# Performance work log

Hardware: AMD Instinct MI355X
Metric: run time of the kernel (lower is better)

## Reference

```python
import jax, jax.numpy as jnp
import numpy as np

B, E, H, C, R = 16, 1024, 1024, 64, 64  # batch, input_size, hidden_size, context_size, context_rank
H4 = 4 * H


def setup_inputs() -> dict:
    key = jax.random.key(0)
    ks = jax.random.split(key, 12)
    n = lambda k, shape, scale: jax.random.normal(k, shape, dtype=jnp.float32) * scale
    return {
        'x': n(ks[0], (B, E), 1.0),
        'h': n(ks[1], (B, H), 1.0),
        'c': n(ks[2], (B, H), 1.0),
        'context': n(ks[3], (B, C), 1.0),
        'Wi': n(ks[4], (E, H4), 0.02),
        'Wi_b': n(ks[5], (H4,), 0.02),
        'Wh': n(ks[6], (H, H4), 0.02),
        'Wh_b': n(ks[7], (H4,), 0.02),
        'AZ_il': n(ks[8], (C, E, R), 0.02),
        'AZ_ir': n(ks[9], (R, H4, C), 0.02),
        'AZ_hl': n(ks[10], (C, H, R), 0.02),
        'AZ_hr': n(ks[11], (R, H4, C), 0.02),
    }


def reference(x, h, c, context, Wi, Wi_b, Wh, Wh_b, AZ_il, AZ_ir, AZ_hl, AZ_hr):
    hs = Wh.shape[0]
    # compute_context_weights: per-sample low-rank weight perturbations
    lhs_i = jnp.einsum('bc,cer->ber', context, AZ_il)      # [B,E,R]
    rhs_i = jnp.einsum('bc,rjc->brj', context, AZ_ir)      # [B,R,4H]
    A_i = jnp.einsum('ber,brj->bej', lhs_i, rhs_i)         # [B,E,4H]
    lhs_h = jnp.einsum('bc,chr->bhr', context, AZ_hl)      # [B,H,R]
    rhs_h = jnp.einsum('bc,rjc->brj', context, AZ_hr)      # [B,R,4H]
    A_h = jnp.einsum('bhr,brj->bhj', lhs_h, rhs_h)         # [B,H,4H]
    # forward (faithful to original: context weights are multiplied by 0)
    Wi_eff = 0.0 * A_i + Wi                                # [B,E,4H]
    Wh_eff = 0.0 * A_h + Wh                                # [B,H,4H]
    ifgo = (jnp.einsum('be,bej->bj', x, Wi_eff) + Wi_b
            + jnp.einsum('bh,bhj->bj', h, Wh_eff) + Wh_b)  # [B,4H]
    i = jax.nn.sigmoid(ifgo[:, :hs])
    f = jax.nn.sigmoid(ifgo[:, hs:2 * hs])
    g = jnp.tanh(ifgo[:, 2 * hs:3 * hs])
    o = jax.nn.sigmoid(ifgo[:, 3 * hs:])
    c_new = f * c + i * g
    h_new = o * jnp.tanh(c_new)
    return (h_new, c_new)
```

## Files before the change

### kernel.cpp

```cpp
#include <hip/hip_runtime.h>
#include <stdint.h>

#define H4_ 4096
#define B_  16

__global__ __launch_bounds__(256) void k1_gemm(
    const float* __restrict__ x, const float* __restrict__ h,
    const float* __restrict__ Wi, const float* __restrict__ Wh,
    float* __restrict__ part, int chunks)
{
    __shared__ float a_lds[256][16];
    __shared__ float red[8][16][32];

    const int ct = blockIdx.x & 127;
    const int s  = blockIdx.x >> 7;
    const int j0 = ct * 32;
    const int t  = threadIdx.x;
    const int c8 = t & 7;
    const int bq = (t >> 3) & 3;
    const int ks = t >> 5;

    float acc[4][4];
    #pragma unroll
    for (int r = 0; r < 4; r++)
        #pragma unroll
        for (int c = 0; c < 4; c++) acc[r][c] = 0.f;

    const int m_beg = s * chunks, m_end = m_beg + chunks;
    for (int m = m_beg; m < m_end; ++m) {
        const float* A  = (m < 4) ? x : h;
        const float* W  = (m < 4) ? Wi : Wh;
        const int    e0 = (m & 3) * 256;

        {
            const int b = t & 15, kc = t >> 4;
            const float* src = A + b * 1024 + e0 + kc * 16;
            float4 v0 = *(const float4*)(src);
            float4 v1 = *(const float4*)(src + 4);
            float4 v2 = *(const float4*)(src + 8);
            float4 v3 = *(const float4*)(src + 12);
            const float vv[16] = { v0.x, v0.y, v0.z, v0.w, v1.x, v1.y, v1.z, v1.w,
                                   v2.x, v2.y, v2.z, v2.w, v3.x, v3.y, v3.z, v3.w };
            #pragma unroll
            for (int j = 0; j < 16; j++) a_lds[kc * 16 + j][b] = vv[j];
        }
        __syncthreads();

        const float* wp = W + (size_t)e0 * H4_ + j0 + c8 * 4;
        #pragma unroll 8
        for (int i = 0; i < 32; i++) {
            const int kl = ks * 32 + i;
            float4 w = *(const float4*)(wp + (size_t)kl * H4_);
            float4 a = *(const float4*)&a_lds[kl][bq * 4];
            acc[0][0] += a.x * w.x; acc[0][1] += a.x * w.y; acc[0][2] += a.x * w.z; acc[0][3] += a.x * w.w;
            acc[1][0] += a.y * w.x; acc[1][1] += a.y * w.y; acc[1][2] += a.y * w.z; acc[1][3] += a.y * w.w;
            acc[2][0] += a.z * w.x; acc[2][1] += a.z * w.y; acc[2][2] += a.z * w.z; acc[2][3] += a.z * w.w;
            acc[3][0] += a.w * w.x; acc[3][1] += a.w * w.y; acc[3][2] += a.w * w.z; acc[3][3] += a.w * w.w;
        }
        __syncthreads();
    }

    #pragma unroll
    for (int r = 0; r < 4; r++)
        *(float4*)&red[ks][bq * 4 + r][c8 * 4] =
            make_float4(acc[r][0], acc[r][1], acc[r][2], acc[r][3]);
    __syncthreads();
    {
        const int b = t >> 4, c = t & 15;
        float s0 = 0.f, s1 = 0.f;
        #pragma unroll
        for (int kk = 0; kk < 8; kk++) {
            s0 += red[kk][b][c];
            s1 += red[kk][b][c + 16];
        }
        float* dst = part + ((size_t)s * B_ + b) * H4_ + j0;
        dst[c]      = s0;
        dst[c + 16] = s1;
    }
}

__global__ __launch_bounds__(256) void k2_act(
    const float* __restrict__ part, const float* __restrict__ c,
    const float* __restrict__ Wi_b, const float* __restrict__ Wh_b,
    float* __restrict__ out, int split)
{
    const int tg = blockIdx.x * 256 + threadIdx.x;
    const int b  = tg >> 10;
    const int j  = tg & 1023;

    float g4[4];
    #pragma unroll
    for (int g = 0; g < 4; g++) {
        const int col = g * 1024 + j;
        float acc = Wi_b[col] + Wh_b[col];
        for (int ss = 0; ss < split; ss++)
            acc += part[((size_t)ss * B_ + b) * H4_ + col];
        g4[g] = acc;
    }
    const float ig = 1.f / (1.f + __expf(-g4[0]));
    const float fg = 1.f / (1.f + __expf(-g4[1]));
    const float gg = tanhf(g4[2]);
    const float og = 1.f / (1.f + __expf(-g4[3]));
    const float cv = c[tg];
    const float cn = fg * cv + ig * gg;
    const float hn = og * tanhf(cn);
    out[tg]         = hn;
    out[16384 + tg] = cn;
}

__global__ __launch_bounds__(256) void k_fused(
    const float* __restrict__ x, const float* __restrict__ h,
    const float* __restrict__ cin,
    const float* __restrict__ Wi, const float* __restrict__ Wh,
    const float* __restrict__ Wi_b, const float* __restrict__ Wh_b,
    float* __restrict__ out)
{
    __shared__ float a_lds[256][16];
    __shared__ float red[16][16][16];
    __shared__ float gate_s[4][16][16];

    const int j0 = blockIdx.x * 16;
    const int t  = threadIdx.x;
    const int ks = t >> 4;
    const int bq = (t >> 2) & 3;
    const int c4 = t & 3;

    float acc[4][4][4];
    #pragma unroll
    for (int g = 0; g < 4; g++)
        #pragma unroll
        for (int r = 0; r < 4; r++)
            #pragma unroll
            for (int c = 0; c < 4; c++) acc[g][r][c] = 0.f;

    for (int m = 0; m < 8; ++m) {
        const float* A  = (m < 4) ? x : h;
        const float* W  = (m < 4) ? Wi : Wh;
        const int    e0 = (m & 3) * 256;
        {
            const int b = t & 15, kc = t >> 4;
            const float* src = A + b * 1024 + e0 + kc * 16;
            float4 v0 = *(const float4*)(src);
            float4 v1 = *(const float4*)(src + 4);
            float4 v2 = *(const float4*)(src + 8);
            float4 v3 = *(const float4*)(src + 12);
            const float vv[16] = { v0.x, v0.y, v0.z, v0.w, v1.x, v1.y, v1.z, v1.w,
                                   v2.x, v2.y, v2.z, v2.w, v3.x, v3.y, v3.z, v3.w };
            #pragma unroll
            for (int jj = 0; jj < 16; jj++) a_lds[kc * 16 + jj][b] = vv[jj];
        }
        __syncthreads();
        #pragma unroll 4
        for (int i = 0; i < 16; i++) {
            const int kl = ks * 16 + i;
            float4 a = *(const float4*)&a_lds[kl][bq * 4];
            const float av[4] = { a.x, a.y, a.z, a.w };
            #pragma unroll
            for (int g = 0; g < 4; g++) {
                float4 w = *(const float4*)(W + (size_t)(e0 + kl) * H4_ + g * 1024 + j0 + c4 * 4);
                #pragma unroll
                for (int r = 0; r < 4; r++) {
                    acc[g][r][0] += av[r] * w.x; acc[g][r][1] += av[r] * w.y;
                    acc[g][r][2] += av[r] * w.z; acc[g][r][3] += av[r] * w.w;
                }
            }
        }
        __syncthreads();
    }

    #pragma unroll
    for (int g = 0; g < 4; g++) {
        #pragma unroll
        for (int r = 0; r < 4; r++)
            *(float4*)&red[ks][bq * 4 + r][c4 * 4] =
                make_float4(acc[g][r][0], acc[g][r][1], acc[g][r][2], acc[g][r][3]);
        __syncthreads();
        {
            const int b = t >> 4, c = t & 15;
            float sum = 0.f;
            #pragma unroll
            for (int kk = 0; kk < 16; kk++) sum += red[kk][b][c];
            gate_s[g][b][c] = sum;
        }
        __syncthreads();
    }

    {
        const int b = t >> 4, jj = t & 15;
        const int j = j0 + jj;
        const float s0 = gate_s[0][b][jj] + Wi_b[j]        + Wh_b[j];
        const float s1 = gate_s[1][b][jj] + Wi_b[1024 + j] + Wh_b[1024 + j];
        const float s2 = gate_s[2][b][jj] + Wi_b[2048 + j] + Wh_b[2048 + j];
        const float s3 = gate_s[3][b][jj] + Wi_b[3072 + j] + Wh_b[3072 + j];
        const float ig = 1.f / (1.f + __expf(-s0));
        const float fg = 1.f / (1.f + __expf(-s1));
        const float gg = tanhf(s2);
        const float og = 1.f / (1.f + __expf(-s3));
        const float cv = cin[b * 1024 + j];
        const float cn = fg * cv + ig * gg;
        const float hn = og * tanhf(cn);
        out[b * 1024 + j]         = hn;
        out[16384 + b * 1024 + j] = cn;
    }
}

extern "C" void kernel_launch(void* const* d_in, const int* in_sizes, int n_in,
                              void* d_out, int out_size, void* d_ws, size_t ws_size,
                              hipStream_t stream) {
    (void)in_sizes; (void)n_in; (void)out_size;
    const float* x    = (const float*)d_in[0];
    const float* h    = (const float*)d_in[1];
    const float* c    = (const float*)d_in[2];
    const float* Wi   = (const float*)d_in[4];
    const float* Wi_b = (const float*)d_in[5];
    const float* Wh   = (const float*)d_in[6];
    const float* Wh_b = (const float*)d_in[7];

    float* part = (float*)d_ws;
    float* out  = (float*)d_out;

    const size_t need1 = (size_t)B_ * H4_ * sizeof(float);
    int split = 0;
    if      (ws_size >= 4 * need1) split = 4;
    else if (ws_size >= 2 * need1) split = 2;
    else if (ws_size >= 1 * need1) split = 1;

    if (split > 0) {
        k1_gemm<<<128 * split, 256, 0, stream>>>(x, h, Wi, Wh, part, 8 / split);
        k2_act<<<64, 256, 0, stream>>>(part, c, Wi_b, Wh_b, out, split);
    } else {
        k_fused<<<64, 256, 0, stream>>>(x, h, c, Wi, Wh, Wi_b, Wh_b, out);
    }
}
```

Measured before the change: 186.1 us.

## Fuse GEMM and LSTM gate activation into one 256-block kernel

Replaces the split-K two-kernel path (partial GEMM sums to workspace, then an activation kernel) with a single fused kernel over 256 blocks. Each block owns 4 hidden columns across all four gates, so the gate nonlinearities and cell update run in-block after an LDS reduction. This removes the workspace round trip and the second launch. In exchange, each block streams the full K=2048 reduction, and each thread reads a 16-byte segment per gate (4 floats per row per gate), which may coalesce less well than before.

```diff
diff --git a/kernel.cpp b/kernel.cpp
--- a/kernel.cpp
+++ b/kernel.cpp
@@ -4,21 +4,23 @@
 #define H4_ 4096
 #define B_  16
 
-__global__ __launch_bounds__(256) void k1_gemm(
+__global__ __launch_bounds__(256) void k_fused2(
     const float* __restrict__ x, const float* __restrict__ h,
+    const float* __restrict__ cin,
     const float* __restrict__ Wi, const float* __restrict__ Wh,
-    float* __restrict__ part, int chunks)
+    const float* __restrict__ Wi_b, const float* __restrict__ Wh_b,
+    float* __restrict__ out)
 {
     __shared__ float a_lds[256][16];
-    __shared__ float red[8][16][32];
+    __shared__ float red[16][16][16];
+    __shared__ float gsum[16][16];
 
-    const int ct = blockIdx.x & 127;
-    const int s  = blockIdx.x >> 7;
-    const int j0 = ct * 32;
+    const int bl = blockIdx.x;
+    const int j0 = (bl & 7) * 128 + (bl >> 3) * 4;
     const int t  = threadIdx.x;
-    const int c8 = t & 7;
-    const int bq = (t >> 3) & 3;
-    const int ks = t >> 5;
+    const int g  = t & 3;
+    const int bq = (t >> 2) & 3;
+    const int ks = t >> 4;
 
     float acc[4][4];
     #pragma unroll
@@ -26,8 +28,7 @@
         #pragma unroll
         for (int c = 0; c < 4; c++) acc[r][c] = 0.f;
 
-    const int m_beg = s * chunks, m_end = m_beg + chunks;
-    for (int m = m_beg; m < m_end; ++m) {
+    for (int m = 0; m < 8; ++m) {
         const float* A  = (m < 4) ? x : h;
         const float* W  = (m < 4) ? Wi : Wh;
         const int    e0 = (m & 3) * 256;
@@ -46,10 +47,10 @@
         }
         __syncthreads();
 
-        const float* wp = W + (size_t)e0 * H4_ + j0 + c8 * 4;
-        #pragma unroll 8
-        for (int i = 0; i < 32; i++) {
-            const int kl = ks * 32 + i;
+        const float* wp = W + (size_t)e0 * H4_ + g * 1024 + j0;
+        #pragma unroll
+        for (int i = 0; i < 16; i++) {
+            const int kl = ks * 16 + i;
             float4 w = *(const float4*)(wp + (size_t)kl * H4_);
             float4 a = *(const float4*)&a_lds[kl][bq * 4];
             acc[0][0] += a.x * w.x; acc[0][1] += a.x * w.y; acc[0][2] += a.x * w.z; acc[0][3] += a.x * w.w;
@@ -62,136 +63,25 @@
 
     #pragma unroll
     for (int r = 0; r < 4; r++)
-        *(float4*)&red[ks][bq * 4 + r][c8 * 4] =
+        *(float4*)&red[ks][bq * 4 + r][g * 4] =
             make_float4(acc[r][0], acc[r][1], acc[r][2], acc[r][3]);
     __syncthreads();
     {
-        const int b = t >> 4, c = t & 15;
-        float s0 = 0.f, s1 = 0.f;
+        const int b = t >> 4, c16 = t & 15;
+        float s = 0.f;
         #pragma unroll
-        for (int kk = 0; kk < 8; kk++) {
-            s0 += red[kk][b][c];
-            s1 += red[kk][b][c + 16];
-        }
-        float* dst = part + ((size_t)s * B_ + b) * H4_ + j0;
-        dst[c]      = s0;
-        dst[c + 16] = s1;
+        for (int kk = 0; kk < 16; kk++) s += red[kk][b][c16];
+        gsum[b][c16] = s;
     }
-}
+    __syncthreads();
 
-__global__ __launch_bounds__(256) void k2_act(
-    const float* __restrict__ part, const float* __restrict__ c,
-    const float* __restrict__ Wi_b, const float* __restrict__ Wh_b,
-    float* __restrict__ out, int split)
-{
-    const int tg = blockIdx.x * 256 + threadIdx.x;
-    const int b  = tg >> 10;
-    const int j  = tg & 1023;
-
-    float g4[4];
-    #pragma unroll
-    for (int g = 0; g < 4; g++) {
-        const int col = g * 1024 + j;
-        float acc = Wi_b[col] + Wh_b[col];
-        for (int ss = 0; ss < split; ss++)
-            acc += part[((size_t)ss * B_ + b) * H4_ + col];
-        g4[g] = acc;
-    }
-    const float ig = 1.f / (1.f + __expf(-g4[0]));
-    const float fg = 1.f / (1.f + __expf(-g4[1]));
-    const float gg = tanhf(g4[2]);
-    const float og = 1.f / (1.f + __expf(-g4[3]));
-    const float cv = c[tg];
-    const float cn = fg * cv + ig * gg;
-    const float hn = og * tanhf(cn);
-    out[tg]         = hn;
-    out[16384 + tg] = cn;
-}
-
-__global__ __launch_bounds__(256) void k_fused(
-    const float* __restrict__ x, const float* __restrict__ h,
-    const float* __restrict__ cin,
-    const float* __restrict__ Wi, const float* __restrict__ Wh,
-    const float* __restrict__ Wi_b, const float* __restrict__ Wh_b,
-    float* __restrict__ out)
-{
-    __shared__ float a_lds[256][16];
-    __shared__ float red[16][16][16];
-    __shared__ float gate_s[4][16][16];
-
-    const int j0 = blockIdx.x * 16;
-    const int t  = threadIdx.x;
-    const int ks = t >> 4;
-    const int bq = (t >> 2) & 3;
-    const int c4 = t & 3;
-
-    float acc[4][4][4];
-    #pragma unroll
-    for (int g = 0; g < 4; g++)
-        #pragma unroll
-        for (int r = 0; r < 4; r++)
-            #pragma unroll
-            for (int c = 0; c < 4; c++) acc[g][r][c] = 0.f;
-
-    for (int m = 0; m < 8; ++m) {
-        const float* A  = (m < 4) ? x : h;
-        const float* W  = (m < 4) ? Wi : Wh;
-        const int    e0 = (m & 3) * 256;
-        {
-            const int b = t & 15, kc = t >> 4;
-            const float* src = A + b * 1024 + e0 + kc * 16;
-            float4 v0 = *(const float4*)(src);
-            float4 v1 = *(const float4*)(src + 4);
-            float4 v2 = *(const float4*)(src + 8);
-            float4 v3 = *(const float4*)(src + 12);
-            const float vv[16] = { v0.x, v0.y, v0.z, v0.w, v1.x, v1.y, v1.z, v1.w,
-                                   v2.x, v2.y, v2.z, v2.w, v3.x, v3.y, v3.z, v3.w };
-            #pragma unroll
-            for (int jj = 0; jj < 16; jj++) a_lds[kc * 16 + jj][b] = vv[jj];
-        }
-        __syncthreads();
-        #pragma unroll 4
-        for (int i = 0; i < 16; i++) {
-            const int kl = ks * 16 + i;
-            float4 a = *(const float4*)&a_lds[kl][bq * 4];
-            const float av[4] = { a.x, a.y, a.z, a.w };
-            #pragma unroll
-            for (int g = 0; g < 4; g++) {
-                float4 w = *(const float4*)(W + (size_t)(e0 + kl) * H4_ + g * 1024 + j0 + c4 * 4);
-                #pragma unroll
-                for (int r = 0; r < 4; r++) {
-                    acc[g][r][0] += av[r] * w.x; acc[g][r][1] += av[r] * w.y;
-                    acc[g][r][2] += av[r] * w.z; acc[g][r][3] += av[r] * w.w;
-                }
-            }
-        }
-        __syncthreads();
-    }
-
-    #pragma unroll
-    for (int g = 0; g < 4; g++) {
-        #pragma unroll
-        for (int r = 0; r < 4; r++)
-            *(float4*)&red[ks][bq * 4 + r][c4 * 4] =
-                make_float4(acc[g][r][0], acc[g][r][1], acc[g][r][2], acc[g][r][3]);
-        __syncthreads();
-        {
-            const int b = t >> 4, c = t & 15;
-            float sum = 0.f;
-            #pragma unroll
-            for (int kk = 0; kk < 16; kk++) sum += red[kk][b][c];
-            gate_s[g][b][c] = sum;
-        }
-        __syncthreads();
-    }
-
-    {
-        const int b = t >> 4, jj = t & 15;
+    if (t < 64) {
+        const int b = t >> 2, jj = t & 3;
         const int j = j0 + jj;
-        const float s0 = gate_s[0][b][jj] + Wi_b[j]        + Wh_b[j];
-        const float s1 = gate_s[1][b][jj] + Wi_b[1024 + j] + Wh_b[1024 + j];
-        const float s2 = gate_s[2][b][jj] + Wi_b[2048 + j] + Wh_b[2048 + j];
-        const float s3 = gate_s[3][b][jj] + Wi_b[3072 + j] + Wh_b[3072 + j];
+        const float s0 = gsum[b][jj]      + Wi_b[j]        + Wh_b[j];
+        const float s1 = gsum[b][4 + jj]  + Wi_b[1024 + j] + Wh_b[1024 + j];
+        const float s2 = gsum[b][8 + jj]  + Wi_b[2048 + j] + Wh_b[2048 + j];
+        const float s3 = gsum[b][12 + jj] + Wi_b[3072 + j] + Wh_b[3072 + j];
         const float ig = 1.f / (1.f + __expf(-s0));
         const float fg = 1.f / (1.f + __expf(-s1));
         const float gg = tanhf(s2);
@@ -207,7 +97,7 @@
 extern "C" void kernel_launch(void* const* d_in, const int* in_sizes, int n_in,
                               void* d_out, int out_size, void* d_ws, size_t ws_size,
                               hipStream_t stream) {
-    (void)in_sizes; (void)n_in; (void)out_size;
+    (void)in_sizes; (void)n_in; (void)out_size; (void)d_ws; (void)ws_size;
     const float* x    = (const float*)d_in[0];
     const float* h    = (const float*)d_in[1];
     const float* c    = (const float*)d_in[2];
@@ -216,19 +106,6 @@
     const float* Wh   = (const float*)d_in[6];
     const float* Wh_b = (const float*)d_in[7];
 
-    float* part = (float*)d_ws;
-    float* out  = (float*)d_out;
-
-    const size_t need1 = (size_t)B_ * H4_ * sizeof(float);
-    int split = 0;
-    if      (ws_size >= 4 * need1) split = 4;
-    else if (ws_size >= 2 * need1) split = 2;
-    else if (ws_size >= 1 * need1) split = 1;
-
-    if (split > 0) {
-        k1_gemm<<<128 * split, 256, 0, stream>>>(x, h, Wi, Wh, part, 8 / split);
-        k2_act<<<64, 256, 0, stream>>>(part, c, Wi_b, Wh_b, out, split);
-    } else {
-        k_fused<<<64, 256, 0, stream>>>(x, h, c, Wi, Wh, Wi_b, Wh_b, out);
-    }
+    k_fused2<<<256, 256, 0, stream>>>(x, h, c, Wi, Wh, Wi_b, Wh_b,
+                                      (float*)d_out);
 }
```

After: 202.3 us. +8.7%, slower.

## Split K eight ways across 1024 blocks and widen fused fallback grid

Applied to the files above, without the earlier changes.

The split-K GEMM now always uses eight K-chunks, one 256-row slab per block, launched as 1024 blocks with the split index in the low bits of blockIdx. This raises parallelism for the memory-bound weight stream, and the activation kernel now sums a fixed, unrolled eight partials. The fused fallback is restructured to 256 blocks of four columns per gate. The cost is a larger workspace requirement (8x partials) and more partial-sum traffic in the second kernel. If the workspace is too small, the code now falls back to the fused kernel instead of using fewer splits.

```diff
diff --git a/kernel.cpp b/kernel.cpp
--- a/kernel.cpp
+++ b/kernel.cpp
@@ -7,13 +7,13 @@
 __global__ __launch_bounds__(256) void k1_gemm(
     const float* __restrict__ x, const float* __restrict__ h,
     const float* __restrict__ Wi, const float* __restrict__ Wh,
-    float* __restrict__ part, int chunks)
+    float* __restrict__ part)
 {
     __shared__ float a_lds[256][16];
     __shared__ float red[8][16][32];
 
-    const int ct = blockIdx.x & 127;
-    const int s  = blockIdx.x >> 7;
+    const int s  = blockIdx.x & 7;
+    const int ct = blockIdx.x >> 3;
     const int j0 = ct * 32;
     const int t  = threadIdx.x;
     const int c8 = t & 7;
@@ -26,38 +26,34 @@
         #pragma unroll
         for (int c = 0; c < 4; c++) acc[r][c] = 0.f;
 
-    const int m_beg = s * chunks, m_end = m_beg + chunks;
-    for (int m = m_beg; m < m_end; ++m) {
-        const float* A  = (m < 4) ? x : h;
-        const float* W  = (m < 4) ? Wi : Wh;
-        const int    e0 = (m & 3) * 256;
-
-        {
-            const int b = t & 15, kc = t >> 4;
-            const float* src = A + b * 1024 + e0 + kc * 16;
-            float4 v0 = *(const float4*)(src);
-            float4 v1 = *(const float4*)(src + 4);
-            float4 v2 = *(const float4*)(src + 8);
-            float4 v3 = *(const float4*)(src + 12);
-            const float vv[16] = { v0.x, v0.y, v0.z, v0.w, v1.x, v1.y, v1.z, v1.w,
-                                   v2.x, v2.y, v2.z, v2.w, v3.x, v3.y, v3.z, v3.w };
-            #pragma unroll
-            for (int j = 0; j < 16; j++) a_lds[kc * 16 + j][b] = vv[j];
-        }
-        __syncthreads();
-
-        const float* wp = W + (size_t)e0 * H4_ + j0 + c8 * 4;
-        #pragma unroll 8
-        for (int i = 0; i < 32; i++) {
-            const int kl = ks * 32 + i;
-            float4 w = *(const float4*)(wp + (size_t)kl * H4_);
-            float4 a = *(const float4*)&a_lds[kl][bq * 4];
-            acc[0][0] += a.x * w.x; acc[0][1] += a.x * w.y; acc[0][2] += a.x * w.z; acc[0][3] += a.x * w.w;
-            acc[1][0] += a.y * w.x; acc[1][1] += a.y * w.y; acc[1][2] += a.y * w.z; acc[1][3] += a.y * w.w;
-            acc[2][0] += a.z * w.x; acc[2][1] += a.z * w.y; acc[2][2] += a.z * w.z; acc[2][3] += a.z * w.w;
-            acc[3][0] += a.w * w.x; acc[3][1] += a.w * w.y; acc[3][2] += a.w * w.z; acc[3][3] += a.w * w.w;
-        }
-        __syncthreads();
+    const float* A  = (s < 4) ? x : h;
+    const float* W  = (s < 4) ? Wi : Wh;
+    const int    e0 = (s & 3) * 256;
+
+    {
+        const int b = t & 15, kc = t >> 4;
+        const float* src = A + b * 1024 + e0 + kc * 16;
+        float4 v0 = *(const float4*)(src);
+        float4 v1 = *(const float4*)(src + 4);
+        float4 v2 = *(const float4*)(src + 8);
+        float4 v3 = *(const float4*)(src + 12);
+        const float vv[16] = { v0.x, v0.y, v0.z, v0.w, v1.x, v1.y, v1.z, v1.w,
+                               v2.x, v2.y, v2.z, v2.w, v3.x, v3.y, v3.z, v3.w };
+        #pragma unroll
+        for (int j = 0; j < 16; j++) a_lds[kc * 16 + j][b] = vv[j];
+    }
+    __syncthreads();
+
+    const float* wp = W + (size_t)e0 * H4_ + j0 + c8 * 4;
+    #pragma unroll 8
+    for (int i = 0; i < 32; i++) {
+        const int kl = ks * 32 + i;
+        float4 w = *(const float4*)(wp + (size_t)kl * H4_);
+        float4 a = *(const float4*)&a_lds[kl][bq * 4];
+        acc[0][0] += a.x * w.x; acc[0][1] += a.x * w.y; acc[0][2] += a.x * w.z; acc[0][3] += a.x * w.w;
+        acc[1][0] += a.y * w.x; acc[1][1] += a.y * w.y; acc[1][2] += a.y * w.z; acc[1][3] += a.y * w.w;
+        acc[2][0] += a.z * w.x; acc[2][1] += a.z * w.y; acc[2][2] += a.z * w.z; acc[2][3] += a.z * w.w;
+        acc[3][0] += a.w * w.x; acc[3][1] += a.w * w.y; acc[3][2] += a.w * w.z; acc[3][3] += a.w * w.w;
     }
 
     #pragma unroll
@@ -82,7 +78,7 @@
 __global__ __launch_bounds__(256) void k2_act(
     const float* __restrict__ part, const float* __restrict__ c,
     const float* __restrict__ Wi_b, const float* __restrict__ Wh_b,
-    float* __restrict__ out, int split)
+    float* __restrict__ out)
 {
     const int tg = blockIdx.x * 256 + threadIdx.x;
     const int b  = tg >> 10;
@@ -93,7 +89,8 @@
     for (int g = 0; g < 4; g++) {
         const int col = g * 1024 + j;
         float acc = Wi_b[col] + Wh_b[col];
-        for (int ss = 0; ss < split; ss++)
+        #pragma unroll
+        for (int ss = 0; ss < 8; ss++)
             acc += part[((size_t)ss * B_ + b) * H4_ + col];
         g4[g] = acc;
     }
@@ -108,7 +105,7 @@
     out[16384 + tg] = cn;
 }
 
-__global__ __launch_bounds__(256) void k_fused(
+__global__ __launch_bounds__(256) void k_fused2(
     const float* __restrict__ x, const float* __restrict__ h,
     const float* __restrict__ cin,
     const float* __restrict__ Wi, const float* __restrict__ Wh,
@@ -117,21 +114,20 @@
 {
     __shared__ float a_lds[256][16];
     __shared__ float red[16][16][16];
-    __shared__ float gate_s[4][16][16];
-
-    const int j0 = blockIdx.x * 16;
+    __shared__ float gsum[16][16];
+
+    const int bl = blockIdx.x;
+    const int j0 = (bl & 7) * 128 + (bl >> 3) * 4;
     const int t  = threadIdx.x;
+    const int g  = t & 3;
+    const int bq = (t >> 2) & 3;
     const int ks = t >> 4;
-    const int bq = (t >> 2) & 3;
-    const int c4 = t & 3;
-
-    float acc[4][4][4];
-    #pragma unroll
-    for (int g = 0; g < 4; g++)
-        #pragma unroll
-        for (int r = 0; r < 4; r++)
-            #pragma unroll
-            for (int c = 0; c < 4; c++) acc[g][r][c] = 0.f;
+
+    float acc[4][4];
+    #pragma unroll
+    for (int r = 0; r < 4; r++)
+        #pragma unroll
+        for (int c = 0; c < 4; c++) acc[r][c] = 0.f;
 
     for (int m = 0; m < 8; ++m) {
         const float* A  = (m < 4) ? x : h;
@@ -150,48 +146,41 @@
             for (int jj = 0; jj < 16; jj++) a_lds[kc * 16 + jj][b] = vv[jj];
         }
         __syncthreads();
+        const float* wp = W + (size_t)e0 * H4_ + g * 1024 + j0;
         #pragma unroll 4
         for (int i = 0; i < 16; i++) {
             const int kl = ks * 16 + i;
+            float4 w = *(const float4*)(wp + (size_t)kl * H4_);
             float4 a = *(const float4*)&a_lds[kl][bq * 4];
-            const float av[4] = { a.x, a.y, a.z, a.w };
-            #pragma unroll
-            for (int g = 0; g < 4; g++) {
-                float4 w = *(const float4*)(W + (size_t)(e0 + kl) * H4_ + g * 1024 + j0 + c4 * 4);
-                #pragma unroll
-                for (int r = 0; r < 4; r++) {
-                    acc[g][r][0] += av[r] * w.x; acc[g][r][1] += av[r] * w.y;
-                    acc[g][r][2] += av[r] * w.z; acc[g][r][3] += av[r] * w.w;
-                }
-            }
+            acc[0][0] += a.x * w.x; acc[0][1] += a.x * w.y; acc[0][2] += a.x * w.z; acc[0][3] += a.x * w.w;
+            acc[1][0] += a.y * w.x; acc[1][1] += a.y * w.y; acc[1][2] += a.y * w.z; acc[1][3] += a.y * w.w;
+            acc[2][0] += a.z * w.x; acc[2][1] += a.z * w.y; acc[2][2] += a.z * w.z; acc[2][3] += a.z * w.w;
+            acc[3][0] += a.w * w.x; acc[3][1] += a.w * w.y; acc[3][2] += a.w * w.z; acc[3][3] += a.w * w.w;
         }
         __syncthreads();
     }
 
     #pragma unroll
-    for (int g = 0; g < 4; g++) {
-        #pragma unroll
-        for (int r = 0; r < 4; r++)
-            *(float4*)&red[ks][bq * 4 + r][c4 * 4] =
-                make_float4(acc[g][r][0], acc[g][r][1], acc[g][r][2], acc[g][r][3]);
-        __syncthreads();
-        {
-            const int b = t >> 4, c = t & 15;
-            float sum = 0.f;
-            #pragma unroll
-            for (int kk = 0; kk < 16; kk++) sum += red[kk][b][c];
-            gate_s[g][b][c] = sum;
-        }
-        __syncthreads();
-    }
-
+    for (int r = 0; r < 4; r++)
+        *(float4*)&red[ks][bq * 4 + r][g * 4] =
+            make_float4(acc[r][0], acc[r][1], acc[r][2], acc[r][3]);
+    __syncthreads();
     {
-        const int b = t >> 4, jj = t & 15;
+        const int b = t >> 4, c16 = t & 15;
+        float sum = 0.f;
+        #pragma unroll
+        for (int kk = 0; kk < 16; kk++) sum += red[kk][b][c16];
+        gsum[b][c16] = sum;
+    }
+    __syncthreads();
+
+    if (t < 64) {
+        const int b = t >> 2, jj = t & 3;
         const int j = j0 + jj;
-        const float s0 = gate_s[0][b][jj] + Wi_b[j]        + Wh_b[j];
-        const float s1 = gate_s[1][b][jj] + Wi_b[1024 + j] + Wh_b[1024 + j];
-        const float s2 = gate_s[2][b][jj] + Wi_b[2048 + j] + Wh_b[2048 + j];
-        const float s3 = gate_s[3][b][jj] + Wi_b[3072 + j] + Wh_b[3072 + j];
+        const float s0 = gsum[b][jj]      + Wi_b[j]        + Wh_b[j];
+        const float s1 = gsum[b][4 + jj]  + Wi_b[1024 + j] + Wh_b[1024 + j];
+        const float s2 = gsum[b][8 + jj]  + Wi_b[2048 + j] + Wh_b[2048 + j];
+        const float s3 = gsum[b][12 + jj] + Wi_b[3072 + j] + Wh_b[3072 + j];
         const float ig = 1.f / (1.f + __expf(-s0));
         const float fg = 1.f / (1.f + __expf(-s1));
         const float gg = tanhf(s2);
@@ -219,16 +208,11 @@
     float* part = (float*)d_ws;
     float* out  = (float*)d_out;
 
-    const size_t need1 = (size_t)B_ * H4_ * sizeof(float);
-    int split = 0;
-    if      (ws_size >= 4 * need1) split = 4;
-    else if (ws_size >= 2 * need1) split = 2;
-    else if (ws_size >= 1 * need1) split = 1;
-
-    if (split > 0) {
-        k1_gemm<<<128 * split, 256, 0, stream>>>(x, h, Wi, Wh, part, 8 / split);
-        k2_act<<<64, 256, 0, stream>>>(part, c, Wi_b, Wh_b, out, split);
+    const size_t need = 8ull * B_ * H4_ * sizeof(float);
+    if (ws_size >= need) {
+        k1_gemm<<<1024, 256, 0, stream>>>(x, h, Wi, Wh, part);
+        k2_act<<<64, 256, 0, stream>>>(part, c, Wi_b, Wh_b, out);
     } else {
-        k_fused<<<64, 256, 0, stream>>>(x, h, c, Wi, Wh, Wi_b, Wh_b, out);
-    }
-}
+        k_fused2<<<64 * 4, 256, 0, stream>>>(x, h, c, Wi, Wh, Wi_b, Wh_b, out);
+    }
+}
```

New measurement: 182.9 us. About the same (-1.7%).
